# Performance work log

Hardware: AMD Instinct MI355X
Metric: run time of the kernel (lower is better)

Reference implementation:

```python
import jax, jax.numpy as jnp
import numpy as np

N = 50000          # padded nodes
E_CFG = 800000     # padded cfg edges
E_GKT = 800000     # padded gkt edges
FN = 128           # node feature dim
FE = 128           # gkt edge feature dim
OUT = 128          # out_size (== hidden dim, required by shared Linears)
HEADS = 8
HEAD = OUT // HEADS
DIN = FN + OUT     # input dim to shared Linears


def _seg_softmax(logits, seg_ids, num_segments):
    mx = jax.ops.segment_max(logits, seg_ids, num_segments=num_segments)
    e = jnp.exp(logits - mx[seg_ids])
    s = jax.ops.segment_sum(e, seg_ids, num_segments=num_segments)
    return e / s[seg_ids]


def setup_inputs() -> dict:
    key = jax.random.key(0)
    ks = jax.random.split(key, 16)
    d = {
        'node_fts': jax.random.normal(ks[0], (N, FN), jnp.float32),
        'gkt_edge_fts': jax.random.normal(ks[1], (E_GKT, FE), jnp.float32),
        'hidden': jax.random.normal(ks[2], (N, OUT), jnp.float32),
        'cfg_indices_padded': jax.random.randint(ks[3], (E_CFG, 2), 0, N, jnp.int32),
        'gkt_indices_padded': jax.random.randint(ks[4], (E_GKT, 2), 0, N, jnp.int32),
    }
    sc = 1.0 / np.sqrt(DIN)
    d['W_m'] = jax.random.normal(ks[5], (DIN, OUT), jnp.float32) * sc
    d['b_m'] = jnp.zeros((OUT,), jnp.float32)
    d['W_skip'] = jax.random.normal(ks[6], (DIN, OUT), jnp.float32) * sc
    d['b_skip'] = jnp.zeros((OUT,), jnp.float32)
    d['W_a1'] = jax.random.normal(ks[7], (DIN, HEADS), jnp.float32) * sc
    d['b_a1'] = jnp.zeros((HEADS,), jnp.float32)
    d['W_a2'] = jax.random.normal(ks[8], (DIN, HEADS), jnp.float32) * sc
    d['b_a2'] = jnp.zeros((HEADS,), jnp.float32)
    d['W_ae'] = jax.random.normal(ks[9], (FE, HEADS), jnp.float32) * (1.0 / np.sqrt(FE))
    d['b_ae'] = jnp.zeros((HEADS,), jnp.float32)
    return d


def reference(node_fts, gkt_edge_fts, hidden, cfg_indices_padded, gkt_indices_padded,
              W_m, b_m, W_skip, b_skip, W_a1, b_a1, W_a2, b_a2, W_ae, b_ae):
    nb_nodes = node_fts.shape[0]
    nb_cfg = cfg_indices_padded.shape[0]
    nb_gkt = gkt_indices_padded.shape[0]
    cfg_row, cfg_col = cfg_indices_padded[:, 0], cfg_indices_padded[:, 1]
    gkt_row, gkt_col = gkt_indices_padded[:, 0], gkt_indices_padded[:, 1]

    # ---- cfg pass ----
    cfg_z = jnp.concatenate([node_fts, hidden], axis=-1)           # [N, DIN]
    cfg_att1 = cfg_z @ W_a1 + b_a1                                 # [N, H]
    cfg_att2 = cfg_z @ W_a2 + b_a2
    cfg_logits = cfg_att1[cfg_row] + cfg_att2[cfg_col]             # [E, H]
    cfg_coefs = _seg_softmax(jax.nn.leaky_relu(cfg_logits), cfg_row, nb_cfg)
    cfg_vals = (cfg_z @ W_m + b_m).reshape(nb_nodes, HEADS, HEAD)  # [N, H, hd]
    cfg_msg = cfg_coefs[:, :, None] * cfg_vals[cfg_col]            # [E, H, hd]
    cfg_hidden = jax.ops.segment_sum(cfg_msg, cfg_row, num_segments=nb_nodes)
    cfg_hidden = cfg_hidden.reshape(nb_nodes, OUT)
    cfg_hidden = cfg_hidden + (cfg_z @ W_skip + b_skip)            # residual
    cfg_hidden = jax.nn.relu(cfg_hidden)

    # ---- gkt pass ----
    gkt_z = jnp.concatenate([node_fts, cfg_hidden], axis=-1)       # [N, DIN]
    gkt_att1 = gkt_z @ W_a1 + b_a1
    gkt_att2 = gkt_z @ W_a2 + b_a2
    gkt_att_e = gkt_edge_fts @ W_ae + b_ae                         # [E, H]
    gkt_logits = gkt_att1[gkt_row] + gkt_att2[gkt_col] + gkt_att_e
    gkt_coefs = _seg_softmax(jax.nn.leaky_relu(gkt_logits), gkt_row, nb_gkt)
    gkt_vals = (gkt_z @ W_m + b_m).reshape(nb_nodes, HEADS, HEAD)
    msg = gkt_coefs[:, :, None] * gkt_vals[gkt_col]
    ret = jax.ops.segment_sum(msg, gkt_row, num_segments=nb_nodes)
    ret = ret.reshape(nb_nodes, OUT)
    ret = ret + (gkt_z @ W_skip + b_skip)
    ret = jax.nn.relu(ret)
    return ret
```

## Files before the change

kernel.cpp:

```cpp
#include <hip/hip_runtime.h>

using short8  = __attribute__((ext_vector_type(8))) short;
using floatx4 = __attribute__((ext_vector_type(4))) float;

#define CAP 64

__device__ __forceinline__ unsigned short f2bf(float f) {
    unsigned int u = __float_as_uint(f);
    u += 0x7fffu + ((u >> 16) & 1u);
    return (unsigned short)(u >> 16);
}
__device__ __forceinline__ float bf2f(unsigned short s) {
    return __uint_as_float(((unsigned int)s) << 16);
}

__global__ void k_prep(const float* __restrict__ Wm, const float* __restrict__ Wsk,
                       const float* __restrict__ Wa1, const float* __restrict__ Wa2,
                       unsigned short* __restrict__ Wpack, float* __restrict__ Wa,
                       const float* __restrict__ nf, const float* __restrict__ hid,
                       unsigned short* __restrict__ zbf,
                       int* __restrict__ cur0, int* __restrict__ cur1, int N) {
    int id = blockIdx.x * 256 + threadIdx.x;
    if (id < 65536) {
        int col = id >> 8;
        int k = id & 255;
        float v = (col < 128) ? Wm[k * 128 + col] : Wsk[k * 128 + (col - 128)];
        Wpack[col * 256 + k] = f2bf(v);
        if (id < 256 * 16) {
            int kk = id >> 4, j = id & 15;
            Wa[kk * 16 + j] = (j < 8) ? Wa1[kk * 8 + j] : Wa2[kk * 8 + (j - 8)];
        }
    }
    if (id < N) { cur0[id] = id * CAP; cur1[id] = id * CAP; }
    if (id >= N * 32) return;
    int row = id >> 5;
    int c4 = (id & 31) * 4;
    float4 av = *(const float4*)&nf[row * 128 + c4];
    float4 bv = *(const float4*)&hid[row * 128 + c4];
    ushort4 pa; pa.x = f2bf(av.x); pa.y = f2bf(av.y); pa.z = f2bf(av.z); pa.w = f2bf(av.w);
    ushort4 pb; pb.x = f2bf(bv.x); pb.y = f2bf(bv.y); pb.z = f2bf(bv.z); pb.w = f2bf(bv.w);
    *(ushort4*)&zbf[row * 256 + c4] = pa;
    *(ushort4*)&zbf[row * 256 + 128 + c4] = pb;
}

__global__ void k_fillw(const int* __restrict__ cfg_idx, const int* __restrict__ gkt_idx,
                        int* __restrict__ cur0, int* __restrict__ cur1,
                        int* __restrict__ ccol0, int* __restrict__ ccol1,
                        int* __restrict__ pos1, const float* __restrict__ att0,
                        float* __restrict__ w0, int Ec, int Eg) {
    int e = blockIdx.x * 256 + threadIdx.x;
    if (e < Ec) {
        int r = cfg_idx[2 * e], c = cfg_idx[2 * e + 1];
        int p = atomicAdd(&cur0[r], 1);
        if (p < r * CAP + CAP) {
            ccol0[p] = c;
            float4 x0 = *(const float4*)&att0[r * 16];
            float4 x1 = *(const float4*)&att0[r * 16 + 4];
            float4 y0 = *(const float4*)&att0[c * 16 + 8];
            float4 y1 = *(const float4*)&att0[c * 16 + 12];
            float l[8] = {x0.x + y0.x, x0.y + y0.y, x0.z + y0.z, x0.w + y0.w,
                          x1.x + y1.x, x1.y + y1.y, x1.z + y1.z, x1.w + y1.w};
            float w[8];
#pragma unroll
            for (int h = 0; h < 8; h++) {
                float ll = (l[h] >= 0.f) ? l[h] : 0.01f * l[h];
                w[h] = __expf(ll);
            }
            float4 wa = {w[0], w[1], w[2], w[3]};
            float4 wb = {w[4], w[5], w[6], w[7]};
            *(float4*)&w0[p * 8] = wa;
            *(float4*)&w0[p * 8 + 4] = wb;
        }
    }
    if (e < Eg) {
        int r = gkt_idx[2 * e], c = gkt_idx[2 * e + 1];
        int p = atomicAdd(&cur1[r], 1);
        if (p < r * CAP + CAP) ccol1[p] = c;
        pos1[e] = p;
    }
}

__launch_bounds__(256)
__global__ void k_wgkt(const float* __restrict__ ef, const float* __restrict__ Wae,
                       const float* __restrict__ bae, const int* __restrict__ gkt_idx,
                       const int* __restrict__ pos1, const float* __restrict__ att1,
                       float* __restrict__ w1, int E) {
    __shared__ float Ws[1024];
    int t = threadIdx.x;
    for (int s = t; s < 1024; s += 256) Ws[s] = Wae[s];
    __syncthreads();
    int e = blockIdx.x * 256 + t;
    if (e >= E) return;
    int p = pos1[e];
    int r = gkt_idx[2 * e], c = gkt_idx[2 * e + 1];
    if (p >= r * CAP + CAP) return;
    float acc[8];
#pragma unroll
    for (int h = 0; h < 8; h++) acc[h] = bae[h];
    const float* row = &ef[(size_t)e * 128];
    for (int k0 = 0; k0 < 128; k0 += 4) {
        float4 v = *(const float4*)&row[k0];
        float vv[4] = {v.x, v.y, v.z, v.w};
#pragma unroll
        for (int rr = 0; rr < 4; rr++) {
            const float* w = &Ws[(k0 + rr) * 8];
#pragma unroll
            for (int h = 0; h < 8; h++) acc[h] += vv[rr] * w[h];
        }
    }
    float4 x0 = *(const float4*)&att1[r * 16];
    float4 x1 = *(const float4*)&att1[r * 16 + 4];
    float4 y0 = *(const float4*)&att1[c * 16 + 8];
    float4 y1 = *(const float4*)&att1[c * 16 + 12];
    float l[8] = {acc[0] + x0.x + y0.x, acc[1] + x0.y + y0.y,
                  acc[2] + x0.z + y0.z, acc[3] + x0.w + y0.w,
                  acc[4] + x1.x + y1.x, acc[5] + x1.y + y1.y,
                  acc[6] + x1.z + y1.z, acc[7] + x1.w + y1.w};
    float w[8];
#pragma unroll
    for (int h = 0; h < 8; h++) {
        float ll = (l[h] >= 0.f) ? l[h] : 0.01f * l[h];
        w[h] = __expf(ll);
    }
    float4 wa = {w[0], w[1], w[2], w[3]};
    float4 wb = {w[4], w[5], w[6], w[7]};
    *(float4*)&w1[p * 8] = wa;
    *(float4*)&w1[p * 8 + 4] = wb;
}

__launch_bounds__(256)
__global__ void k_gemm(const unsigned short* __restrict__ zbf,
                       const unsigned short* __restrict__ Wpack,
                       const float* __restrict__ bm, const float* __restrict__ bsk,
                       unsigned short* __restrict__ vals, float* __restrict__ skip, int M) {
    const int colblk = blockIdx.x;
    const int rowBase = blockIdx.y * 128;
    __shared__ short As[128 * 40];
    __shared__ short Bs[128 * 40];
    const int t = threadIdx.x;
    const int wid = t >> 6, lane = t & 63;
    const int wm = wid >> 1, wn = wid & 1;

    floatx4 acc[4][4];
#pragma unroll
    for (int i = 0; i < 4; i++)
#pragma unroll
        for (int j = 0; j < 4; j++) acc[i][j] = (floatx4){0.f, 0.f, 0.f, 0.f};

    const unsigned short* Bbase = Wpack + colblk * 128 * 256;
    const int kq = (lane >> 4) * 8;
    const int rr = lane & 15;

    for (int kt = 0; kt < 256; kt += 32) {
#pragma unroll
        for (int s = 0; s < 2; s++) {
            int ch = t + s * 256;
            int r = ch >> 2, c = ch & 3;
            int gr = rowBase + r; if (gr >= M) gr = M - 1;
            *(int4*)&As[r * 40 + c * 8] = *(const int4*)&zbf[gr * 256 + kt + c * 8];
            *(int4*)&Bs[r * 40 + c * 8] = *(const int4*)&Bbase[r * 256 + kt + c * 8];
        }
        __syncthreads();
        short8 af[4], bfm[4];
#pragma unroll
        for (int i = 0; i < 4; i++) af[i] = *(short8*)&As[(wm * 64 + i * 16 + rr) * 40 + kq];
#pragma unroll
        for (int j = 0; j < 4; j++) bfm[j] = *(short8*)&Bs[(wn * 64 + j * 16 + rr) * 40 + kq];
#pragma unroll
        for (int i = 0; i < 4; i++)
#pragma unroll
            for (int j = 0; j < 4; j++)
                acc[i][j] = __builtin_amdgcn_mfma_f32_16x16x32_bf16(af[i], bfm[j], acc[i][j], 0, 0, 0);
        __syncthreads();
    }

    const int rquad = lane >> 4, cidx = lane & 15;
#pragma unroll
    for (int i = 0; i < 4; i++) {
#pragma unroll
        for (int j = 0; j < 4; j++) {
            int gc = wn * 64 + j * 16 + cidx;
#pragma unroll
            for (int r = 0; r < 4; r++) {
                int gr = rowBase + wm * 64 + i * 16 + rquad * 4 + r;
                if (gr < M) {
                    float v = acc[i][j][r];
                    if (colblk == 0) vals[gr * 128 + gc] = f2bf(v + bm[gc]);
                    else             skip[gr * 128 + gc] = v + bsk[gc];
                }
            }
        }
    }
}

__launch_bounds__(256)
__global__ void k_att(const float* __restrict__ zA, const float* __restrict__ zB,
                      const float* __restrict__ Wa, const float* __restrict__ ba1,
                      const float* __restrict__ ba2, float* __restrict__ att, int N) {
    __shared__ float Ws[4096];
    int t = threadIdx.x;
#pragma unroll
    for (int s = 0; s < 16; s++) Ws[s * 256 + t] = Wa[s * 256 + t];
    __syncthreads();
    int node = blockIdx.x * 256 + t;
    if (node >= N) return;
    float acc[16];
#pragma unroll
    for (int j = 0; j < 16; j++) acc[j] = (j < 8) ? ba1[j] : ba2[j - 8];
    const float* a = &zA[node * 128];
    const float* b = &zB[node * 128];
    for (int k0 = 0; k0 < 128; k0 += 4) {
        float4 v = *(const float4*)&a[k0];
        float vv[4] = {v.x, v.y, v.z, v.w};
#pragma unroll
        for (int r = 0; r < 4; r++) {
            const float* w = &Ws[(k0 + r) * 16];
#pragma unroll
            for (int j = 0; j < 16; j++) acc[j] += vv[r] * w[j];
        }
    }
    for (int k0 = 0; k0 < 128; k0 += 4) {
        float4 v = *(const float4*)&b[k0];
        float vv[4] = {v.x, v.y, v.z, v.w};
#pragma unroll
        for (int r = 0; r < 4; r++) {
            const float* w = &Ws[(128 + k0 + r) * 16];
#pragma unroll
            for (int j = 0; j < 16; j++) acc[j] += vv[r] * w[j];
        }
    }
#pragma unroll
    for (int j = 0; j < 16; j++) att[node * 16 + j] = acc[j];
}

template <int PHASE>
__launch_bounds__(256)
__global__ void k_agg(const int* __restrict__ cursor, const int* __restrict__ ccol,
                      const float* __restrict__ wbuf,
                      const unsigned short* __restrict__ vals,
                      const float* __restrict__ skip,
                      unsigned short* __restrict__ zbf, float* __restrict__ cfgh,
                      float* __restrict__ out, int N) {
    int node = (blockIdx.x * 256 + threadIdx.x) >> 6;
    int lane = threadIdx.x & 63;
    if (node >= N) return;
    int h = lane >> 3;
    int f0 = lane * 2;
    int base = node * CAP;
    int cnt = cursor[node] - base;
    if (cnt > CAP) cnt = CAP;
    if (cnt < 0) cnt = 0;

    int mycol = 0;
    if (lane < cnt) mycol = ccol[base + lane];
    const float* wrow = &wbuf[base * 8 + h];
    float acc0 = 0.f, acc1 = 0.f, dsum = 0.f;
#pragma unroll 4
    for (int s = 0; s < cnt; s++) {
        int col = __shfl(mycol, s);
        float w = wrow[s * 8];
        unsigned int pv = *(const unsigned int*)&vals[col * 128 + f0];
        acc0 += w * bf2f((unsigned short)(pv & 0xffffu));
        acc1 += w * bf2f((unsigned short)(pv >> 16));
        dsum += w;
    }
    if (cnt > 0) {
        float inv = 1.f / dsum;
        acc0 *= inv; acc1 *= inv;
    }
    float r0 = acc0 + skip[node * 128 + f0];
    float r1 = acc1 + skip[node * 128 + f0 + 1];
    r0 = r0 > 0.f ? r0 : 0.f;
    r1 = r1 > 0.f ? r1 : 0.f;
    if (PHASE == 0) {
        unsigned int packed = ((unsigned int)f2bf(r1) << 16) | (unsigned int)f2bf(r0);
        *(unsigned int*)&zbf[node * 256 + 128 + f0] = packed;
        float2 fo = {r0, r1};
        *(float2*)&cfgh[node * 128 + f0] = fo;
    } else {
        float2 fo = {r0, r1};
        *(float2*)&out[node * 128 + f0] = fo;
    }
}

extern "C" void kernel_launch(void* const* d_in, const int* in_sizes, int n_in,
                              void* d_out, int out_size, void* d_ws, size_t ws_size,
                              hipStream_t stream) {
    const float* node_fts = (const float*)d_in[0];
    const float* gkt_ef   = (const float*)d_in[1];
    const float* hidden   = (const float*)d_in[2];
    const int*   cfg_idx  = (const int*)d_in[3];
    const int*   gkt_idx  = (const int*)d_in[4];
    const float* W_m  = (const float*)d_in[5];
    const float* b_m  = (const float*)d_in[6];
    const float* W_sk = (const float*)d_in[7];
    const float* b_sk = (const float*)d_in[8];
    const float* W_a1 = (const float*)d_in[9];
    const float* b_a1 = (const float*)d_in[10];
    const float* W_a2 = (const float*)d_in[11];
    const float* b_a2 = (const float*)d_in[12];
    const float* W_ae = (const float*)d_in[13];
    const float* b_ae = (const float*)d_in[14];

    const int N  = in_sizes[0] / 128;
    const int Ec = in_sizes[3] / 2;
    const int Eg = in_sizes[4] / 2;
    const int Emax = (Ec > Eg) ? Ec : Eg;

    char* ws = (char*)d_ws;
    size_t off = 0;
    auto alloc = [&](size_t bytes) -> void* {
        off = (off + 255) & ~(size_t)255;
        void* p = ws + off;
        off += bytes;
        return p;
    };
    unsigned short* zbf   = (unsigned short*)alloc((size_t)N * 256 * 2);
    unsigned short* vals  = (unsigned short*)alloc((size_t)N * 128 * 2);
    float* skip   = (float*)alloc((size_t)N * 128 * 4);
    float* cfgh   = (float*)alloc((size_t)N * 128 * 4);
    float* att    = (float*)alloc((size_t)N * 16 * 4);
    unsigned short* Wpack = (unsigned short*)alloc(256 * 256 * 2);
    float* Wa     = (float*)alloc(256 * 16 * 4);
    int* cur0     = (int*)alloc((size_t)N * 4);
    int* cur1     = (int*)alloc((size_t)N * 4);
    int* ccol0    = (int*)alloc((size_t)N * CAP * 4);
    int* ccol1    = (int*)alloc((size_t)N * CAP * 4);
    int* pos1     = (int*)alloc((size_t)Eg * 4);
    float* w0     = (float*)alloc((size_t)N * CAP * 8 * 4);
    float* w1     = (float*)alloc((size_t)N * CAP * 8 * 4);

    dim3 ggrid(2, (N + 127) / 128);

    k_prep<<<(N * 32 + 255) / 256, 256, 0, stream>>>(W_m, W_sk, W_a1, W_a2, Wpack, Wa,
                                                     node_fts, hidden, zbf, cur0, cur1, N);
    k_att<<<(N + 255) / 256, 256, 0, stream>>>(node_fts, hidden, Wa, b_a1, b_a2, att, N);
    k_fillw<<<(Emax + 255) / 256, 256, 0, stream>>>(cfg_idx, gkt_idx, cur0, cur1,
                                                    ccol0, ccol1, pos1, att, w0, Ec, Eg);

    k_gemm<<<ggrid, 256, 0, stream>>>(zbf, Wpack, b_m, b_sk, vals, skip, N);
    k_agg<0><<<(N * 64 + 255) / 256, 256, 0, stream>>>(cur0, ccol0, w0, vals, skip,
                                                       zbf, cfgh, nullptr, N);

    k_att<<<(N + 255) / 256, 256, 0, stream>>>(node_fts, cfgh, Wa, b_a1, b_a2, att, N);
    k_wgkt<<<(Eg + 255) / 256, 256, 0, stream>>>(gkt_ef, W_ae, b_ae, gkt_idx, pos1,
                                                 att, w1, Eg);
    k_gemm<<<ggrid, 256, 0, stream>>>(zbf, Wpack, b_m, b_sk, vals, skip, N);
    k_agg<1><<<(N * 64 + 255) / 256, 256, 0, stream>>>(cur1, ccol1, w1, vals, skip,
                                                       nullptr, nullptr, (float*)d_out, N);
}
```

Baseline: 1.009 ms.

## Fuse gkt attention projection into cfg aggregation and coalesce edge-feature projection

The first k_att launch now also saves the node_fts half of the attention projection (attA). The cfg aggregation kernel then finishes each node's gkt attention logits with a wave-wide shuffle reduction, which removes the second k_att launch and the fp32 cfg_hidden buffer round trip. k_wgkt is rewritten as a grid-stride kernel in which 32 lanes share one edge row, with coalesced nontemporal loads, weights held in registers and a shuffle reduction. The final output uses nontemporal stores. In exchange the aggregation kernel does extra shuffle reductions, and the edge kernel spends more instructions per edge on reductions.

```diff
diff --git a/kernel.cpp b/kernel.cpp
--- a/kernel.cpp
+++ b/kernel.cpp
@@ -2,6 +2,7 @@
 
 using short8  = __attribute__((ext_vector_type(8))) short;
 using floatx4 = __attribute__((ext_vector_type(4))) float;
+using floatx2 = __attribute__((ext_vector_type(2))) float;
 
 #define CAP 64
 
@@ -84,48 +85,49 @@
 __global__ void k_wgkt(const float* __restrict__ ef, const float* __restrict__ Wae,
                        const float* __restrict__ bae, const int* __restrict__ gkt_idx,
                        const int* __restrict__ pos1, const float* __restrict__ att1,
-                       float* __restrict__ w1, int E) {
-    __shared__ float Ws[1024];
-    int t = threadIdx.x;
-    for (int s = t; s < 1024; s += 256) Ws[s] = Wae[s];
-    __syncthreads();
-    int e = blockIdx.x * 256 + t;
-    if (e >= E) return;
-    int p = pos1[e];
-    int r = gkt_idx[2 * e], c = gkt_idx[2 * e + 1];
-    if (p >= r * CAP + CAP) return;
-    float acc[8];
-#pragma unroll
-    for (int h = 0; h < 8; h++) acc[h] = bae[h];
-    const float* row = &ef[(size_t)e * 128];
-    for (int k0 = 0; k0 < 128; k0 += 4) {
-        float4 v = *(const float4*)&row[k0];
-        float vv[4] = {v.x, v.y, v.z, v.w};
-#pragma unroll
-        for (int rr = 0; rr < 4; rr++) {
-            const float* w = &Ws[(k0 + rr) * 8];
-#pragma unroll
-            for (int h = 0; h < 8; h++) acc[h] += vv[rr] * w[h];
-        }
-    }
-    float4 x0 = *(const float4*)&att1[r * 16];
-    float4 x1 = *(const float4*)&att1[r * 16 + 4];
-    float4 y0 = *(const float4*)&att1[c * 16 + 8];
-    float4 y1 = *(const float4*)&att1[c * 16 + 12];
-    float l[8] = {acc[0] + x0.x + y0.x, acc[1] + x0.y + y0.y,
-                  acc[2] + x0.z + y0.z, acc[3] + x0.w + y0.w,
-                  acc[4] + x1.x + y1.x, acc[5] + x1.y + y1.y,
-                  acc[6] + x1.z + y1.z, acc[7] + x1.w + y1.w};
-    float w[8];
-#pragma unroll
-    for (int h = 0; h < 8; h++) {
-        float ll = (l[h] >= 0.f) ? l[h] : 0.01f * l[h];
-        w[h] = __expf(ll);
-    }
-    float4 wa = {w[0], w[1], w[2], w[3]};
-    float4 wb = {w[4], w[5], w[6], w[7]};
-    *(float4*)&w1[p * 8] = wa;
-    *(float4*)&w1[p * 8 + 4] = wb;
+                       float* __restrict__ w1, int E, int nGroups) {
+    const int lane = threadIdx.x & 63;
+    const int wv = threadIdx.x >> 6;
+    const int sub = lane & 31;
+    floatx4 wr[8];
+#pragma unroll
+    for (int r = 0; r < 4; r++) {
+        wr[2 * r]     = *(const floatx4*)&Wae[(sub * 4 + r) * 8];
+        wr[2 * r + 1] = *(const floatx4*)&Wae[(sub * 4 + r) * 8 + 4];
+    }
+    for (int g = blockIdx.x; g < nGroups; g += gridDim.x) {
+        int e = g * 8 + wv * 2 + (lane >> 5);
+        int eL = (e < E) ? e : (E - 1);
+        floatx4 v = __builtin_nontemporal_load(
+                        (const floatx4*)&ef[(size_t)eL * 128 + sub * 4]);
+        float acc[8];
+#pragma unroll
+        for (int j = 0; j < 8; j++) acc[j] = 0.f;
+        float vv0 = v[0], vv1 = v[1], vv2 = v[2], vv3 = v[3];
+#pragma unroll
+        for (int j = 0; j < 4; j++) {
+            acc[j]     += vv0 * wr[0][j] + vv1 * wr[2][j] + vv2 * wr[4][j] + vv3 * wr[6][j];
+            acc[j + 4] += vv0 * wr[1][j] + vv1 * wr[3][j] + vv2 * wr[5][j] + vv3 * wr[7][j];
+        }
+#pragma unroll
+        for (int d = 1; d <= 16; d <<= 1) {
+#pragma unroll
+            for (int j = 0; j < 8; j++) acc[j] += __shfl_xor(acc[j], d);
+        }
+        if (sub < 8 && e < E) {
+            int h = sub;
+            float ae = acc[0];
+#pragma unroll
+            for (int j = 1; j < 8; j++) ae = (h == j) ? acc[j] : ae;
+            int p = pos1[e];
+            int r = gkt_idx[2 * e], c = gkt_idx[2 * e + 1];
+            if (p < r * CAP + CAP) {
+                float logit = ae + bae[h] + att1[r * 16 + h] + att1[c * 16 + 8 + h];
+                float ll = (logit >= 0.f) ? logit : 0.01f * logit;
+                w1[p * 8 + h] = __expf(ll);
+            }
+        }
+    }
 }
 
 __launch_bounds__(256)
@@ -196,7 +198,8 @@
 __launch_bounds__(256)
 __global__ void k_att(const float* __restrict__ zA, const float* __restrict__ zB,
                       const float* __restrict__ Wa, const float* __restrict__ ba1,
-                      const float* __restrict__ ba2, float* __restrict__ att, int N) {
+                      const float* __restrict__ ba2, float* __restrict__ att,
+                      float* __restrict__ attA, int N) {
     __shared__ float Ws[4096];
     int t = threadIdx.x;
 #pragma unroll
@@ -219,6 +222,8 @@
             for (int j = 0; j < 16; j++) acc[j] += vv[r] * w[j];
         }
     }
+#pragma unroll
+    for (int j = 0; j < 16; j++) attA[node * 16 + j] = acc[j];
     for (int k0 = 0; k0 < 128; k0 += 4) {
         float4 v = *(const float4*)&b[k0];
         float vv[4] = {v.x, v.y, v.z, v.w};
@@ -239,7 +244,8 @@
                       const float* __restrict__ wbuf,
                       const unsigned short* __restrict__ vals,
                       const float* __restrict__ skip,
-                      unsigned short* __restrict__ zbf, float* __restrict__ cfgh,
+                      const float* __restrict__ Wa, const float* __restrict__ attA,
+                      unsigned short* __restrict__ zbf, float* __restrict__ att1,
                       float* __restrict__ out, int N) {
     int node = (blockIdx.x * 256 + threadIdx.x) >> 6;
     int lane = threadIdx.x & 63;
@@ -275,11 +281,31 @@
     if (PHASE == 0) {
         unsigned int packed = ((unsigned int)f2bf(r1) << 16) | (unsigned int)f2bf(r0);
         *(unsigned int*)&zbf[node * 256 + 128 + f0] = packed;
-        float2 fo = {r0, r1};
-        *(float2*)&cfgh[node * 128 + f0] = fo;
+        float p[16];
+        {
+            const floatx4* wr = (const floatx4*)&Wa[(128 + f0) * 16];
+            floatx4 a0 = wr[0], a1 = wr[1], a2 = wr[2], a3 = wr[3];
+            floatx4 b0 = wr[4], b1 = wr[5], b2 = wr[6], b3 = wr[7];
+#pragma unroll
+            for (int q = 0; q < 4; q++) {
+                p[0 + q]  = r0 * a0[q] + r1 * b0[q];
+                p[4 + q]  = r0 * a1[q] + r1 * b1[q];
+                p[8 + q]  = r0 * a2[q] + r1 * b2[q];
+                p[12 + q] = r0 * a3[q] + r1 * b3[q];
+            }
+        }
+#pragma unroll
+        for (int d = 1; d < 64; d <<= 1) {
+#pragma unroll
+            for (int j = 0; j < 16; j++) p[j] += __shfl_xor(p[j], d);
+        }
+        float rsel = p[0];
+#pragma unroll
+        for (int j = 1; j < 16; j++) rsel = (lane == j) ? p[j] : rsel;
+        if (lane < 16) att1[node * 16 + lane] = attA[node * 16 + lane] + rsel;
     } else {
-        float2 fo = {r0, r1};
-        *(float2*)&out[node * 128 + f0] = fo;
+        floatx2 fo = {r0, r1};
+        __builtin_nontemporal_store(fo, (floatx2*)&out[node * 128 + f0]);
     }
 }
 
@@ -318,8 +344,8 @@
     unsigned short* zbf   = (unsigned short*)alloc((size_t)N * 256 * 2);
     unsigned short* vals  = (unsigned short*)alloc((size_t)N * 128 * 2);
     float* skip   = (float*)alloc((size_t)N * 128 * 4);
-    float* cfgh   = (float*)alloc((size_t)N * 128 * 4);
     float* att    = (float*)alloc((size_t)N * 16 * 4);
+    float* attA   = (float*)alloc((size_t)N * 16 * 4);
     unsigned short* Wpack = (unsigned short*)alloc(256 * 256 * 2);
     float* Wa     = (float*)alloc(256 * 16 * 4);
     int* cur0     = (int*)alloc((size_t)N * 4);
@@ -331,21 +357,24 @@
     float* w1     = (float*)alloc((size_t)N * CAP * 8 * 4);
 
     dim3 ggrid(2, (N + 127) / 128);
+    const int nGroups = (Eg + 7) / 8;
+    int wgktBlocks = 8192; if (wgktBlocks > nGroups) wgktBlocks = nGroups;
 
     k_prep<<<(N * 32 + 255) / 256, 256, 0, stream>>>(W_m, W_sk, W_a1, W_a2, Wpack, Wa,
                                                      node_fts, hidden, zbf, cur0, cur1, N);
-    k_att<<<(N + 255) / 256, 256, 0, stream>>>(node_fts, hidden, Wa, b_a1, b_a2, att, N);
+    k_att<<<(N + 255) / 256, 256, 0, stream>>>(node_fts, hidden, Wa, b_a1, b_a2,
+                                               att, attA, N);
     k_fillw<<<(Emax + 255) / 256, 256, 0, stream>>>(cfg_idx, gkt_idx, cur0, cur1,
                                                     ccol0, ccol1, pos1, att, w0, Ec, Eg);
 
     k_gemm<<<ggrid, 256, 0, stream>>>(zbf, Wpack, b_m, b_sk, vals, skip, N);
     k_agg<0><<<(N * 64 + 255) / 256, 256, 0, stream>>>(cur0, ccol0, w0, vals, skip,
-                                                       zbf, cfgh, nullptr, N);
-
-    k_att<<<(N + 255) / 256, 256, 0, stream>>>(node_fts, cfgh, Wa, b_a1, b_a2, att, N);
-    k_wgkt<<<(Eg + 255) / 256, 256, 0, stream>>>(gkt_ef, W_ae, b_ae, gkt_idx, pos1,
-                                                 att, w1, Eg);
+                                                       Wa, attA, zbf, att, nullptr, N);
+
+    k_wgkt<<<wgktBlocks, 256, 0, stream>>>(gkt_ef, W_ae, b_ae, gkt_idx, pos1,
+                                           att, w1, Eg, nGroups);
     k_gemm<<<ggrid, 256, 0, stream>>>(zbf, Wpack, b_m, b_sk, vals, skip, N);
     k_agg<1><<<(N * 64 + 255) / 256, 256, 0, stream>>>(cur1, ccol1, w1, vals, skip,
-                                                       nullptr, nullptr, (float*)d_out, N);
-}
+                                                       nullptr, nullptr, nullptr, nullptr,
+                                                       (float*)d_out, N);
+}
```

New measurement: 1.031 ms. 1.02x slower.
